# Performance work log

Measured on AMD Instinct MI355X. Metric: run time of the kernel, lower is better.

The kernel has to match this reference:

```python
import jax, jax.numpy as jnp
import numpy as np

ALPHA = 0.35  # dual-cone bonus weight (recall() default)
EPS = 1e-12   # matches F.normalize default eps behavior closely enough in fp32

N_CUBES = 131072
EMBED_DIM = 384
BATCH = 1024


def _l2norm(x):
    # F.normalize(x, dim=-1)
    n = jnp.sqrt(jnp.sum(x * x, axis=-1, keepdims=True))
    return x / jnp.maximum(n, EPS)


def setup_inputs() -> dict:
    key = jax.random.key(0)
    k1, k2, k3 = jax.random.split(key, 3)
    query = jax.random.normal(k1, (BATCH, EMBED_DIM), dtype=jnp.float32)
    # bake() stores normalized primal; dual = normalize(primal + 0.05*randn)
    primal = _l2norm(jax.random.normal(k2, (N_CUBES, EMBED_DIM), dtype=jnp.float32))
    pert = jax.random.normal(k3, (N_CUBES, EMBED_DIM), dtype=jnp.float32) * 0.05
    dual = _l2norm(primal + pert)
    return {
        "query": query,
        "embeddings": primal,
        "dual_vectors": dual,
        "top_k": 16,
    }


def reference(query, embeddings, dual_vectors, top_k):
    """Vectorized CubeChain.recall over a batch of queries.

    score[b, i] = cos(q_b, emb_i) + ALPHA * max(0, cos(q_b, dual_i))
    Returns (top-k scores descending, top-k cube indices) per query.
    """
    q = _l2norm(query)              # [B, D]
    e = _l2norm(embeddings)         # [N, D]
    d = _l2norm(dual_vectors)       # [N, D]
    primal_cos = jnp.einsum("bd,nd->bn", q, e)              # [B, N]
    dual_fit = jnp.maximum(jnp.einsum("bd,nd->bn", q, d), 0.0)
    scores = primal_cos + ALPHA * dual_fit                   # [B, N]
    top_vals, top_idx = jax.lax.top_k(scores, top_k)         # descending sort + slice
    return top_vals, top_idx
```

## Files before the change

### kernel.cpp

```cpp
#include <hip/hip_runtime.h>

#define ALPHA 0.35f
#define BQ 1024
#define DIM 384
#define NC 131072
#define TOPK 16

#define QT 128
#define NQT (BQ / QT)
#define CH 512
#define NCH (NC / CH)
#define SUBC 64
#define NSUB (CH / SUBC)
#define BK 64
#define NKI (DIM / BK)
#define ASTR 72

typedef short bf16x8 __attribute__((ext_vector_type(8)));
typedef float floatx4 __attribute__((ext_vector_type(4)));
typedef unsigned long long ull;
typedef unsigned int u32;

static __device__ __forceinline__ unsigned pk2(float a, float b) {
  unsigned ua = __builtin_bit_cast(unsigned, a);
  unsigned ub = __builtin_bit_cast(unsigned, b);
  return __builtin_amdgcn_perm(ub, ua, 0x07060302u);
}

static __device__ __forceinline__ void stage_half(const float* __restrict__ src,
                                                  ushort* __restrict__ dst) {
  const float4* p = reinterpret_cast<const float4*>(src);
  float4 v0 = p[0], v1 = p[1], v2 = p[2], v3 = p[3];
  float4 v4 = p[4], v5 = p[5], v6 = p[6], v7 = p[7];
  uint4* q = reinterpret_cast<uint4*>(dst);
  q[0] = make_uint4(pk2(v0.x, v0.y), pk2(v0.z, v0.w), pk2(v1.x, v1.y), pk2(v1.z, v1.w));
  q[1] = make_uint4(pk2(v2.x, v2.y), pk2(v2.z, v2.w), pk2(v3.x, v3.y), pk2(v3.z, v3.w));
  q[2] = make_uint4(pk2(v4.x, v4.y), pk2(v4.z, v4.w), pk2(v5.x, v5.y), pk2(v5.z, v5.w));
  q[3] = make_uint4(pk2(v6.x, v6.y), pk2(v6.z, v6.w), pk2(v7.x, v7.y), pk2(v7.z, v7.w));
}

static __device__ __forceinline__ void ce_asc(ull& a, ull& b) {
  ull lo = b < a ? b : a;
  ull hi = b < a ? a : b;
  a = lo; b = hi;
}
static __device__ __forceinline__ void ce_desc(ull& a, ull& b) {
  ull lo = b < a ? b : a;
  ull hi = b < a ? a : b;
  a = hi; b = lo;
}
static __device__ __forceinline__ void sort16_asc(ull* B) {
  #pragma unroll
  for (int k = 2; k <= 16; k <<= 1) {
    #pragma unroll
    for (int j = k >> 1; j > 0; j >>= 1) {
      #pragma unroll
      for (int i = 0; i < 16; i++) {
        int l = i ^ j;
        if (l > i) {
          if ((i & k) == 0) ce_asc(B[i], B[l]);
          else              ce_desc(B[i], B[l]);
        }
      }
    }
  }
}
static __device__ __forceinline__ void merge_desc16(ull* H) {
  #pragma unroll
  for (int j = 8; j > 0; j >>= 1) {
    #pragma unroll
    for (int i = 0; i < 16; i++) {
      int l = i ^ j;
      if (l > i) ce_desc(H[i], H[l]);
    }
  }
}

__global__ __launch_bounds__(384) void qnorm_kernel(const float* __restrict__ q,
                                                    float* __restrict__ qn) {
  const int b = blockIdx.x;
  const int t = threadIdx.x;
  float v = q[b * DIM + t];
  float s = v * v;
  #pragma unroll
  for (int m = 32; m; m >>= 1) s += __shfl_xor(s, m);
  __shared__ float ws[6];
  if ((t & 63) == 0) ws[t >> 6] = s;
  __syncthreads();
  float tot = ws[0] + ws[1] + ws[2] + ws[3] + ws[4] + ws[5];
  float n = fmaxf(sqrtf(tot), 1e-12f);
  qn[b * DIM + t] = v / n;
}

__global__ __launch_bounds__(256) void rownorm_kernel(const float* __restrict__ e,
                                                      const float* __restrict__ d,
                                                      float* __restrict__ inv_e,
                                                      float* __restrict__ inv_d) {
  const int wid = threadIdx.x >> 6, lane = threadIdx.x & 63;
  const int row = blockIdx.x * 4 + wid;
  const float* src = blockIdx.y ? d : e;
  const float* p = src + (size_t)row * DIM;
  float s = 0.f;
  #pragma unroll
  for (int j = 0; j < 6; j++) { float v = p[j * 64 + lane]; s += v * v; }
  #pragma unroll
  for (int m = 32; m; m >>= 1) s += __shfl_xor(s, m);
  if (lane == 0) {
    float n = fmaxf(sqrtf(s), 1e-12f);
    (blockIdx.y ? inv_d : inv_e)[row] = 1.0f / n;
  }
}

__global__ __launch_bounds__(256, 3) void score_kernel(
    const float* __restrict__ e, const float* __restrict__ d,
    const float* __restrict__ qn, const float* __restrict__ inv_e,
    const float* __restrict__ inv_d, float* __restrict__ cand_vals,
    int* __restrict__ cand_idx) {
  __shared__ __align__(16) char smem[36864];
  ushort* As = (ushort*)smem;
  ushort* Bs = (ushort*)(smem + 18432);
  float*  sc = (float*)smem;

  const int t = threadIdx.x;
  const int qt = blockIdx.x, ch = blockIdx.y;
  const int q0 = qt * QT;
  const int c0 = ch * CH;
  const int lane = t & 63, wave = t >> 6;
  const int wy = wave >> 1, wx = wave & 1;
  const int mrow = lane & 15, quad = lane >> 4;

  const int q = t & 127;
  const int h = t >> 7;

  const int srow = t >> 1, shalf = t & 1;
  const float* qsrc = qn + (size_t)(q0 + srow) * DIM + shalf * 32;
  const float* bsel = (srow & 1) ? d : e;

  ull H[16];
  #pragma unroll
  for (int i = 0; i < 16; i++) H[i] = 0ull;

  for (int sub = 0; sub < NSUB; sub++) {
    const int cb = c0 + sub * SUBC;
    const float* bsrc = bsel + (size_t)(cb + (srow >> 1)) * DIM + shalf * 32;
    floatx4 acc[4][4];
    #pragma unroll
    for (int i = 0; i < 4; i++)
      #pragma unroll
      for (int j = 0; j < 4; j++) acc[i][j] = (floatx4)0.f;

    for (int ki = 0; ki < NKI; ki++) {
      const int kb = ki * BK;
      __syncthreads();
      stage_half(qsrc + kb, &As[srow * ASTR + shalf * 32]);
      stage_half(bsrc + kb, &Bs[srow * ASTR + shalf * 32]);
      __syncthreads();
      #pragma unroll
      for (int ks = 0; ks < 2; ks++) {
        bf16x8 af[4], bf[4];
        #pragma unroll
        for (int i = 0; i < 4; i++)
          af[i] = *reinterpret_cast<const bf16x8*>(&As[(wy * 64 + i * 16 + mrow) * ASTR + ks * 32 + quad * 8]);
        #pragma unroll
        for (int j = 0; j < 4; j++)
          bf[j] = *reinterpret_cast<const bf16x8*>(&Bs[(wx * 64 + j * 16 + mrow) * ASTR + ks * 32 + quad * 8]);
        #pragma unroll
        for (int i = 0; i < 4; i++)
          #pragma unroll
          for (int j = 0; j < 4; j++)
            acc[i][j] = __builtin_amdgcn_mfma_f32_16x16x32_bf16(af[i], bf[j], acc[i][j], 0, 0, 0);
      }
    }
    __syncthreads();
    {
      const int col = lane & 15;
      #pragma unroll
      for (int j = 0; j < 4; j++) {
        const int candl = wx * 32 + j * 8 + (col >> 1);
        const int cg = cb + candl;
        const float ie = inv_e[cg];
        const float id = inv_d[cg];
        #pragma unroll
        for (int i = 0; i < 4; i++) {
          #pragma unroll
          for (int r = 0; r < 4; r++) {
            float v = acc[i][j][r];
            float p = __shfl_xor(v, 1);
            if (!(col & 1)) {
              float s = v * ie + ALPHA * fmaxf(p * id, 0.f);
              sc[(wy * 64 + i * 16 + quad * 4 + r) * 65 + candl] = s;
            }
          }
        }
      }
    }
    __syncthreads();
    #pragma unroll
    for (int b = 0; b < 2; b++) {
      ull Bk[16];
      #pragma unroll
      for (int j = 0; j < 16; j++) {
        const int c = h * 32 + b * 16 + j;
        float s = sc[q * 65 + c];
        u32 u = __builtin_bit_cast(u32, s);
        u32 m = (u & 0x80000000u) ? ~u : (u | 0x80000000u);
        Bk[j] = ((ull)m << 32) | (u32)~(u32)(cb + c);
      }
      sort16_asc(Bk);
      #pragma unroll
      for (int i = 0; i < 16; i++) H[i] = H[i] >= Bk[i] ? H[i] : Bk[i];
      merge_desc16(H);
    }
  }

  __syncthreads();
  u32* scu = (u32*)smem;
  if (h == 1) {
    #pragma unroll
    for (int i = 0; i < 16; i++) {
      scu[q * 65 + i]      = (u32)(H[i] >> 32);
      scu[q * 65 + 16 + i] = (u32)H[i];
    }
  }
  __syncthreads();
  if (h == 0) {
    #pragma unroll
    for (int i = 0; i < 16; i++) {
      ull o = ((ull)scu[q * 65 + (15 - i)] << 32) | scu[q * 65 + 16 + (15 - i)];
      H[i] = H[i] >= o ? H[i] : o;
    }
    merge_desc16(H);
    const int qg = q0 + q;
    const size_t base = ((size_t)ch * BQ + qg) * TOPK;
    #pragma unroll
    for (int i = 0; i < 16; i++) {
      u32 m = (u32)(H[i] >> 32);
      u32 u = (m & 0x80000000u) ? (m & 0x7fffffffu) : ~m;
      cand_vals[base + i] = __builtin_bit_cast(float, u);
      cand_idx[base + i] = (int)~(u32)H[i];
    }
  }
}

#define POOL (NCH * TOPK)
#define MSEL 32
__global__ __launch_bounds__(256) void merge_rescore_kernel(
    const float* __restrict__ cand_vals, const int* __restrict__ cand_idx,
    const float* __restrict__ qn, const float* __restrict__ e,
    const float* __restrict__ d, const float* __restrict__ inv_e,
    const float* __restrict__ inv_d, float* __restrict__ out) {
  __shared__ float mv[POOL];
  __shared__ int   mi[POOL];
  __shared__ float qf[DIM];
  __shared__ float wrv[4]; __shared__ int wri[4]; __shared__ int wrp[4];
  __shared__ float selv[MSEL]; __shared__ int seli[MSEL];
  __shared__ float fv[MSEL]; __shared__ int fi[MSEL];

  const int q = blockIdx.x, t = threadIdx.x;
  const int lane = t & 63, wave = t >> 6;

  #pragma unroll
  for (int j = 0; j < POOL / 256; j++) {
    int el = t + 256 * j;
    mv[el] = cand_vals[((size_t)(el >> 4) * BQ + q) * TOPK + (el & 15)];
    mi[el] = cand_idx[((size_t)(el >> 4) * BQ + q) * TOPK + (el & 15)];
  }
  if (t < 128) { qf[t] = qn[q * DIM + t]; qf[t + 128] = qn[q * DIM + t + 128]; qf[t + 256] = qn[q * DIM + t + 256]; }
  __syncthreads();

  for (int pass = 0; pass < MSEL; pass++) {
    float bv = -INFINITY; int bi = 0x7fffffff, bp = 0;
    #pragma unroll
    for (int j = 0; j < POOL / 256; j++) {
      int el = t + 256 * j;
      float v = mv[el]; int ix = mi[el];
      if (v > bv || (v == bv && ix < bi)) { bv = v; bi = ix; bp = el; }
    }
    #pragma unroll
    for (int off = 1; off < 64; off <<= 1) {
      float ov = __shfl_xor(bv, off); int oi = __shfl_xor(bi, off); int op = __shfl_xor(bp, off);
      if (ov > bv || (ov == bv && oi < bi)) { bv = ov; bi = oi; bp = op; }
    }
    if (lane == 0) { wrv[wave] = bv; wri[wave] = bi; wrp[wave] = bp; }
    __syncthreads();
    if (t == 0) {
      float xv = wrv[0]; int xi = wri[0], xp = wrp[0];
      #pragma unroll
      for (int w = 1; w < 4; w++) {
        if (wrv[w] > xv || (wrv[w] == xv && wri[w] < xi)) { xv = wrv[w]; xi = wri[w]; xp = wrp[w]; }
      }
      selv[pass] = xv; seli[pass] = xi;
      mv[xp] = -INFINITY; mi[xp] = 0x7fffffff;
    }
    __syncthreads();
  }

  for (int c = wave; c < MSEL; c += 4) {
    int idx = seli[c];
    const float* er = e + (size_t)idx * DIM;
    const float* dr = d + (size_t)idx * DIM;
    float se = 0.f, sd = 0.f;
    #pragma unroll
    for (int j = 0; j < 6; j++) {
      float qv = qf[j * 64 + lane];
      se += qv * er[j * 64 + lane];
      sd += qv * dr[j * 64 + lane];
    }
    #pragma unroll
    for (int off = 32; off; off >>= 1) { se += __shfl_xor(se, off); sd += __shfl_xor(sd, off); }
    if (lane == 0) {
      fv[c] = se * inv_e[idx] + ALPHA * fmaxf(sd * inv_d[idx], 0.f);
      fi[c] = idx;
    }
  }
  __syncthreads();

  if (t == 0) {
    unsigned used = 0u;
    for (int p = 0; p < TOPK; p++) {
      float bv = -INFINITY; int bi = 0x7fffffff, bp = 0;
      for (int c = 0; c < MSEL; c++) {
        if (used & (1u << c)) continue;
        float v = fv[c]; int ix = fi[c];
        if (v > bv || (v == bv && ix < bi)) { bv = v; bi = ix; bp = c; }
      }
      used |= (1u << bp);
      out[q * TOPK + p] = bv;
      out[BQ * TOPK + q * TOPK + p] = (float)bi;
    }
  }
}

extern "C" void kernel_launch(void* const* d_in, const int* in_sizes, int n_in,
                              void* d_out, int out_size, void* d_ws, size_t ws_size,
                              hipStream_t stream) {
  const float* q = (const float*)d_in[0];
  const float* e = (const float*)d_in[1];
  const float* d = (const float*)d_in[2];

  float* ws = (float*)d_ws;
  float* qn        = ws;
  float* inv_e     = qn + BQ * DIM;
  float* inv_d     = inv_e + NC;
  float* cand_vals = inv_d + NC;
  int*   cand_idx  = (int*)(cand_vals + (size_t)NCH * BQ * TOPK);
  float* out = (float*)d_out;

  qnorm_kernel<<<BQ, 384, 0, stream>>>(q, qn);
  rownorm_kernel<<<dim3(NC / 4, 2), 256, 0, stream>>>(e, d, inv_e, inv_d);
  score_kernel<<<dim3(NQT, NCH), 256, 0, stream>>>(e, d, qn, inv_e, inv_d, cand_vals, cand_idx);
  merge_rescore_kernel<<<BQ, 256, 0, stream>>>(cand_vals, cand_idx, qn, e, d, inv_e, inv_d, out);
}
```

Before: 1.733 ms.

## Pre-convert inputs to bf16 and double-buffer async global-to-LDS loads in score kernel

```diff
diff --git a/kernel.cpp b/kernel.cpp
--- a/kernel.cpp
+++ b/kernel.cpp
@@ -14,29 +14,31 @@
 #define NSUB (CH / SUBC)
 #define BK 64
 #define NKI (DIM / BK)
-#define ASTR 72
+#define NROUND (NSUB * NKI)
 
 typedef short bf16x8 __attribute__((ext_vector_type(8)));
 typedef float floatx4 __attribute__((ext_vector_type(4)));
 typedef unsigned long long ull;
 typedef unsigned int u32;
 
+#define AS1 __attribute__((address_space(1)))
+#define AS3 __attribute__((address_space(3)))
+
 static __device__ __forceinline__ unsigned pk2(float a, float b) {
   unsigned ua = __builtin_bit_cast(unsigned, a);
   unsigned ub = __builtin_bit_cast(unsigned, b);
   return __builtin_amdgcn_perm(ub, ua, 0x07060302u);
 }
 
-static __device__ __forceinline__ void stage_half(const float* __restrict__ src,
-                                                  ushort* __restrict__ dst) {
-  const float4* p = reinterpret_cast<const float4*>(src);
-  float4 v0 = p[0], v1 = p[1], v2 = p[2], v3 = p[3];
-  float4 v4 = p[4], v5 = p[5], v6 = p[6], v7 = p[7];
-  uint4* q = reinterpret_cast<uint4*>(dst);
-  q[0] = make_uint4(pk2(v0.x, v0.y), pk2(v0.z, v0.w), pk2(v1.x, v1.y), pk2(v1.z, v1.w));
-  q[1] = make_uint4(pk2(v2.x, v2.y), pk2(v2.z, v2.w), pk2(v3.x, v3.y), pk2(v3.z, v3.w));
-  q[2] = make_uint4(pk2(v4.x, v4.y), pk2(v4.z, v4.w), pk2(v5.x, v5.y), pk2(v5.z, v5.w));
-  q[3] = make_uint4(pk2(v6.x, v6.y), pk2(v6.z, v6.w), pk2(v7.x, v7.y), pk2(v7.z, v7.w));
+static __device__ __forceinline__ void gl16(const char* g, const char* l) {
+  __builtin_amdgcn_global_load_lds((const AS1 unsigned int*)(unsigned long long)g,
+                                   (AS3 unsigned int*)(unsigned long long)l, 16, 0, 0);
+}
+
+static __device__ __forceinline__ void bar() {
+  asm volatile("" ::: "memory");
+  __builtin_amdgcn_s_barrier();
+  asm volatile("" ::: "memory");
 }
 
 static __device__ __forceinline__ void ce_asc(ull& a, ull& b) {
@@ -77,7 +79,8 @@
 }
 
 __global__ __launch_bounds__(384) void qnorm_kernel(const float* __restrict__ q,
-                                                    float* __restrict__ qn) {
+                                                    float* __restrict__ qn,
+                                                    ushort* __restrict__ qn16) {
   const int b = blockIdx.x;
   const int t = threadIdx.x;
   float v = q[b * DIM + t];
@@ -89,17 +92,21 @@
   __syncthreads();
   float tot = ws[0] + ws[1] + ws[2] + ws[3] + ws[4] + ws[5];
   float n = fmaxf(sqrtf(tot), 1e-12f);
-  qn[b * DIM + t] = v / n;
-}
-
-__global__ __launch_bounds__(256) void rownorm_kernel(const float* __restrict__ e,
+  float vn = v / n;
+  qn[b * DIM + t] = vn;
+  float vn1 = __shfl_down(vn, 1);
+  if (!(t & 1)) ((u32*)qn16)[b * (DIM / 2) + (t >> 1)] = pk2(vn, vn1);
+}
+
+__global__ __launch_bounds__(256) void convert_kernel(const float* __restrict__ e,
                                                       const float* __restrict__ d,
                                                       float* __restrict__ inv_e,
-                                                      float* __restrict__ inv_d) {
+                                                      float* __restrict__ inv_d,
+                                                      ushort* __restrict__ ed16) {
   const int wid = threadIdx.x >> 6, lane = threadIdx.x & 63;
-  const int row = blockIdx.x * 4 + wid;
-  const float* src = blockIdx.y ? d : e;
-  const float* p = src + (size_t)row * DIM;
+  const int g = blockIdx.x * 4 + wid;
+  const int cube = g >> 1, sel = g & 1;
+  const float* p = (sel ? d : e) + (size_t)cube * DIM;
   float s = 0.f;
   #pragma unroll
   for (int j = 0; j < 6; j++) { float v = p[j * 64 + lane]; s += v * v; }
@@ -107,24 +114,30 @@
   for (int m = 32; m; m >>= 1) s += __shfl_xor(s, m);
   if (lane == 0) {
     float n = fmaxf(sqrtf(s), 1e-12f);
-    (blockIdx.y ? inv_d : inv_e)[row] = 1.0f / n;
-  }
-}
-
-__global__ __launch_bounds__(256, 3) void score_kernel(
-    const float* __restrict__ e, const float* __restrict__ d,
-    const float* __restrict__ qn, const float* __restrict__ inv_e,
-    const float* __restrict__ inv_d, float* __restrict__ cand_vals,
-    int* __restrict__ cand_idx) {
-  __shared__ __align__(16) char smem[36864];
-  ushort* As = (ushort*)smem;
-  ushort* Bs = (ushort*)(smem + 18432);
-  float*  sc = (float*)smem;
+    (sel ? inv_d : inv_e)[cube] = 1.0f / n;
+  }
+  u32* dst = (u32*)(ed16 + (size_t)g * DIM);
+  #pragma unroll
+  for (int j = 0; j < 3; j++) {
+    float2 w = *(const float2*)(p + j * 128 + 2 * lane);
+    dst[j * 64 + lane] = pk2(w.x, w.y);
+  }
+}
+
+__global__ __launch_bounds__(256, 2) void score_kernel(
+    const ushort* __restrict__ ed16, const ushort* __restrict__ qn16,
+    const float* __restrict__ inv_e, const float* __restrict__ inv_d,
+    float* __restrict__ cand_vals, int* __restrict__ cand_idx) {
+  __shared__ __align__(16) char smem[65536];
 
   const int t = threadIdx.x;
-  const int qt = blockIdx.x, ch = blockIdx.y;
+  const int bid = blockIdx.x;
+  const int x8 = bid & 7, jj8 = bid >> 3;
+  const int ch = x8 + 8 * (jj8 >> 3);
+  const int qt = jj8 & 7;
   const int q0 = qt * QT;
   const int c0 = ch * CH;
+
   const int lane = t & 63, wave = t >> 6;
   const int wy = wave >> 1, wx = wave & 1;
   const int mrow = lane & 15, quad = lane >> 4;
@@ -132,54 +145,98 @@
   const int q = t & 127;
   const int h = t >> 7;
 
-  const int srow = t >> 1, shalf = t & 1;
-  const float* qsrc = qn + (size_t)(q0 + srow) * DIM + shalf * 32;
-  const float* bsel = (srow & 1) ? d : e;
+  const int sr8 = lane >> 3, ss = lane & 7;
+  u32 offRow[4];
+  #pragma unroll
+  for (int k = 0; k < 4; k++) {
+    int row = k * 32 + wave * 8 + sr8;
+    offRow[k] = (u32)row * 768u + (u32)((ss ^ sr8) * 16);
+  }
+  const u32 ldsW = (u32)wave * 1024u;
+
+  u32 aoff[4], boff[4], sks[2];
+  #pragma unroll
+  for (int i = 0; i < 4; i++) aoff[i] = (u32)(wy * 64 + i * 16 + mrow) * 128u;
+  #pragma unroll
+  for (int j = 0; j < 4; j++) boff[j] = (u32)(wx * 64 + j * 16 + mrow) * 128u;
+  #pragma unroll
+  for (int ks = 0; ks < 2; ks++) sks[ks] = (u32)(((ks * 4 + quad) ^ (mrow & 7)) * 16);
+
+  const char* qbase = (const char*)qn16 + (size_t)q0 * 768;
+  const char* ebase = (const char*)ed16 + (size_t)(c0 * 2) * 768;
+
+  auto STAGE = [&](int buf, int ssub, int ski) {
+    const char* aS = qbase + (size_t)ski * 128;
+    const char* bS = ebase + (size_t)(ssub * 128) * 768 + (size_t)ski * 128;
+    const char* lb = smem + (u32)buf * 32768u + ldsW;
+    #pragma unroll
+    for (int k = 0; k < 4; k++) {
+      gl16(aS + offRow[k], lb + k * 4096u);
+      gl16(bS + offRow[k], lb + 16384u + k * 4096u);
+    }
+  };
+
+  float* sc = (float*)(smem + 32768);
 
   ull H[16];
   #pragma unroll
   for (int i = 0; i < 16; i++) H[i] = 0ull;
+
+  STAGE(0, 0, 0);
 
   for (int sub = 0; sub < NSUB; sub++) {
     const int cb = c0 + sub * SUBC;
-    const float* bsrc = bsel + (size_t)(cb + (srow >> 1)) * DIM + shalf * 32;
+    float ie[4], id[4];
+    #pragma unroll
+    for (int j = 0; j < 4; j++) {
+      int cg = cb + wx * 32 + j * 8 + (mrow >> 1);
+      ie[j] = inv_e[cg]; id[j] = inv_d[cg];
+    }
     floatx4 acc[4][4];
     #pragma unroll
     for (int i = 0; i < 4; i++)
       #pragma unroll
       for (int j = 0; j < 4; j++) acc[i][j] = (floatx4)0.f;
 
+    #pragma unroll
     for (int ki = 0; ki < NKI; ki++) {
-      const int kb = ki * BK;
-      __syncthreads();
-      stage_half(qsrc + kb, &As[srow * ASTR + shalf * 32]);
-      stage_half(bsrc + kb, &Bs[srow * ASTR + shalf * 32]);
-      __syncthreads();
+      const int rr = sub * NKI + ki;
+      if (!(sub == NSUB - 1 && ki == NKI - 1)) {
+        const int nsub = (ki == NKI - 1) ? sub + 1 : sub;
+        const int nki  = (ki == NKI - 1) ? 0 : ki + 1;
+        STAGE((rr + 1) & 1, nsub, nki);
+        asm volatile("s_waitcnt vmcnt(8)" ::: "memory");
+      } else {
+        asm volatile("s_waitcnt vmcnt(0)" ::: "memory");
+      }
+      bar();
+      const char* Ab = smem + (u32)(rr & 1) * 32768u;
+      const char* Bb = Ab + 16384;
       #pragma unroll
       for (int ks = 0; ks < 2; ks++) {
         bf16x8 af[4], bf[4];
         #pragma unroll
         for (int i = 0; i < 4; i++)
-          af[i] = *reinterpret_cast<const bf16x8*>(&As[(wy * 64 + i * 16 + mrow) * ASTR + ks * 32 + quad * 8]);
+          af[i] = *reinterpret_cast<const bf16x8*>(Ab + aoff[i] + sks[ks]);
         #pragma unroll
         for (int j = 0; j < 4; j++)
-          bf[j] = *reinterpret_cast<const bf16x8*>(&Bs[(wx * 64 + j * 16 + mrow) * ASTR + ks * 32 + quad * 8]);
+          bf[j] = *reinterpret_cast<const bf16x8*>(Bb + boff[j] + sks[ks]);
+        __builtin_amdgcn_s_setprio(1);
         #pragma unroll
         for (int i = 0; i < 4; i++)
           #pragma unroll
           for (int j = 0; j < 4; j++)
             acc[i][j] = __builtin_amdgcn_mfma_f32_16x16x32_bf16(af[i], bf[j], acc[i][j], 0, 0, 0);
-      }
-    }
-    __syncthreads();
+        __builtin_amdgcn_s_setprio(0);
+      }
+      bar();
+    }
+
     {
       const int col = lane & 15;
       #pragma unroll
       for (int j = 0; j < 4; j++) {
         const int candl = wx * 32 + j * 8 + (col >> 1);
-        const int cg = cb + candl;
-        const float ie = inv_e[cg];
-        const float id = inv_d[cg];
         #pragma unroll
         for (int i = 0; i < 4; i++) {
           #pragma unroll
@@ -187,8 +244,9 @@
             float v = acc[i][j][r];
             float p = __shfl_xor(v, 1);
             if (!(col & 1)) {
-              float s = v * ie + ALPHA * fmaxf(p * id, 0.f);
-              sc[(wy * 64 + i * 16 + quad * 4 + r) * 65 + candl] = s;
+              const int qrow = wy * 64 + i * 16 + quad * 4 + r;
+              float s = v * ie[j] + ALPHA * fmaxf(p * id[j], 0.f);
+              sc[qrow * 64 + (candl ^ (qrow & 31))] = s;
             }
           }
         }
@@ -201,7 +259,7 @@
       #pragma unroll
       for (int j = 0; j < 16; j++) {
         const int c = h * 32 + b * 16 + j;
-        float s = sc[q * 65 + c];
+        float s = sc[q * 64 + (c ^ (q & 31))];
         u32 u = __builtin_bit_cast(u32, s);
         u32 m = (u & 0x80000000u) ? ~u : (u | 0x80000000u);
         Bk[j] = ((ull)m << 32) | (u32)~(u32)(cb + c);
@@ -211,22 +269,23 @@
       for (int i = 0; i < 16; i++) H[i] = H[i] >= Bk[i] ? H[i] : Bk[i];
       merge_desc16(H);
     }
-  }
-
-  __syncthreads();
-  u32* scu = (u32*)smem;
+    __syncthreads();
+  }
+
+  u32* scu = (u32*)(smem + 32768);
   if (h == 1) {
     #pragma unroll
     for (int i = 0; i < 16; i++) {
-      scu[q * 65 + i]      = (u32)(H[i] >> 32);
-      scu[q * 65 + 16 + i] = (u32)H[i];
+      scu[q * 64 + (i ^ (q & 31))]        = (u32)(H[i] >> 32);
+      scu[q * 64 + ((16 + i) ^ (q & 31))] = (u32)H[i];
     }
   }
   __syncthreads();
   if (h == 0) {
     #pragma unroll
     for (int i = 0; i < 16; i++) {
-      ull o = ((ull)scu[q * 65 + (15 - i)] << 32) | scu[q * 65 + 16 + (15 - i)];
+      ull o = ((ull)scu[q * 64 + ((15 - i) ^ (q & 31))] << 32) |
+              scu[q * 64 + ((31 - i) ^ (q & 31))];
       H[i] = H[i] >= o ? H[i] : o;
     }
     merge_desc16(H);
@@ -344,10 +403,12 @@
   float* inv_d     = inv_e + NC;
   float* cand_vals = inv_d + NC;
   int*   cand_idx  = (int*)(cand_vals + (size_t)NCH * BQ * TOPK);
+  ushort* qn16     = (ushort*)(cand_idx + (size_t)NCH * BQ * TOPK);
+  ushort* ed16     = qn16 + (size_t)BQ * DIM;
   float* out = (float*)d_out;
 
-  qnorm_kernel<<<BQ, 384, 0, stream>>>(q, qn);
-  rownorm_kernel<<<dim3(NC / 4, 2), 256, 0, stream>>>(e, d, inv_e, inv_d);
-  score_kernel<<<dim3(NQT, NCH), 256, 0, stream>>>(e, d, qn, inv_e, inv_d, cand_vals, cand_idx);
+  qnorm_kernel<<<BQ, 384, 0, stream>>>(q, qn, qn16);
+  convert_kernel<<<NC * 2 / 4, 256, 0, stream>>>(e, d, inv_e, inv_d, ed16);
+  score_kernel<<<NQT * NCH, 256, 0, stream>>>(ed16, qn16, inv_e, inv_d, cand_vals, cand_idx);
   merge_rescore_kernel<<<BQ, 256, 0, stream>>>(cand_vals, cand_idx, qn, e, d, inv_e, inv_d, out);
 }
```

New measurement: 1.598 ms. 7.8% less time.
